# Optimization experiments

Measured on AMD Instinct MI355X. Metric: run time of the kernel, lower is better.

Reference implementation:

```python
import jax, jax.numpy as jnp
import numpy as np

EMBED = 8      # == n_qubits, forced by x[:, i, :].view(batch, n_qubits)
FFN = 4096
B, S = 32, 2048


def setup_inputs() -> dict:
    key = jax.random.key(0)
    k_x, k_t, k_w1, k_b1, k_w2, k_b2 = jax.random.split(key, 6)
    x = jax.random.normal(k_x, (B, S, EMBED), dtype=jnp.float32)
    theta = jax.random.normal(k_t, (), dtype=jnp.float32)  # shared trainable RY angle
    # torch.nn.Linear-style init bounds
    lim1 = 1.0 / np.sqrt(EMBED)
    lim2 = 1.0 / np.sqrt(FFN)
    W1 = jax.random.uniform(k_w1, (FFN, EMBED), jnp.float32, -lim1, lim1)
    b1 = jax.random.uniform(k_b1, (FFN,), jnp.float32, -lim1, lim1)
    W2 = jax.random.uniform(k_w2, (EMBED, FFN), jnp.float32, -lim2, lim2)
    b2 = jax.random.uniform(k_b2, (EMBED,), jnp.float32, -lim2, lim2)
    return {"x": x, "theta": theta, "W1": W1, "b1": b1, "W2": W2, "b2": b2}


def reference(x, theta, W1, b1, W2, b2):
    # Quantum circuit, solved analytically (product state, single-qubit gates):
    # |0> --RX(x_i)--RY(theta)--> <Z_i> = cos(theta) * cos(x_i)
    # This fuses the original per-token Python loop into one elementwise op.
    q = jnp.cos(theta) * jnp.cos(x)                 # [B, S, 8]
    # dropout is identity in eval mode
    h = jax.nn.relu(jnp.einsum('bsk,fk->bsf', q, W1) + b1)   # [B, S, FFN]
    out = jnp.einsum('bsf,ef->bse', h, W2) + b2              # [B, S, 8]
    return out
```

## Files before the change

kernel.cpp:

```cpp
#include <hip/hip_runtime.h>
#include <math.h>

#define FFN_DIM 4096
#define NCHUNK  128

typedef _Float16 f16x8 __attribute__((ext_vector_type(8)));
typedef __fp16   h16x2 __attribute__((ext_vector_type(2)));
typedef float    f32x16 __attribute__((ext_vector_type(16)));
typedef float    f32x4  __attribute__((ext_vector_type(4)));

__global__ void build_frags_kernel(const float* __restrict__ w1,
                                   const float* __restrict__ b1,
                                   const float* __restrict__ w2,
                                   _Float16* __restrict__ w1f,
                                   _Float16* __restrict__ w2f) {
    int i = blockIdx.x * 256 + threadIdx.x;
    if (i < NCHUNK * 64 * 8) {
        int j    = i & 7;
        int lane = (i >> 3) & 63;
        int cc   = i >> 9;
        _Float16 v;
        if (lane < 32) v = (_Float16)w1[(cc * 32 + lane) * 8 + j];
        else           v = (j == 0) ? (_Float16)b1[cc * 32 + (lane & 31)]
                                    : (_Float16)0.0f;
        w1f[i] = v;
    }
    if (i < NCHUNK * 2 * 16 * 8) {
        int j  = i & 7;
        int ci = (i >> 3) & 15;
        int c  = (i >> 7) & 1;
        int cc = i >> 8;
        int g = ci >> 3, e = ci & 7;
        int k = 8 * g + j;
        int fl = (k & 3) + 8 * ((k >> 2) & 1) + 4 * (k >> 3);
        int f = 32 * cc + 16 * c + fl;
        w2f[i] = (_Float16)w2[e * FFN_DIM + f];
    }
}

__global__ __launch_bounds__(256, 6) void ffq_mfma_kernel(
    const float* __restrict__ x,
    const float* __restrict__ theta,
    const _Float16* __restrict__ w1f,
    const _Float16* __restrict__ w2f,
    const float* __restrict__ b2,
    float* __restrict__ out,
    int n_tok)
{
    __shared__ float part[4][64][4];

    const int tid  = threadIdx.x;
    const int lane = tid & 63;
    const int wave = tid >> 6;
    const int l31  = lane & 31;
    const int g    = lane >> 5;

    const int tb = blockIdx.x * 32;
    const float cth = cosf(theta[0]);

    f16x8 bq = {};
    if (g == 0) {
        int tok = tb + l31;
        int rt = tok < n_tok ? tok : (n_tok - 1);
        const f32x4* xp = (const f32x4*)(x + (size_t)rt * 8);
        f32x4 x0 = xp[0], x1 = xp[1];
        bq[0] = (_Float16)(cth * cosf(x0.x));
        bq[1] = (_Float16)(cth * cosf(x0.y));
        bq[2] = (_Float16)(cth * cosf(x0.z));
        bq[3] = (_Float16)(cth * cosf(x0.w));
        bq[4] = (_Float16)(cth * cosf(x1.x));
        bq[5] = (_Float16)(cth * cosf(x1.y));
        bq[6] = (_Float16)(cth * cosf(x1.z));
        bq[7] = (_Float16)(cth * cosf(x1.w));
    } else {
        bq[0] = (_Float16)1.0f;
    }

    f32x16 acc = {};
    const f32x16 zero16 = {};

    const int  ci   = g * 8 + (l31 & 7);
    const _Float16* a1p = w1f + (size_t)lane * 8;
    const _Float16* a2p = w2f + (size_t)ci * 8;

    union U8 { f16x8 v; h16x2 p[4]; };
    const h16x2 hz = {(__fp16)0.0f, (__fp16)0.0f};

    const int c0 = wave * (NCHUNK / 4);
    const int c1 = c0 + (NCHUNK / 4);

    #pragma unroll 2
    for (int cc = c0; cc < c1; ++cc) {
        f16x8 A1  = *(const f16x8*)(a1p + (size_t)cc * 512);
        f16x8 A2a = *(const f16x8*)(a2p + (size_t)cc * 256);
        f16x8 A2b = *(const f16x8*)(a2p + (size_t)cc * 256 + 128);

        f32x16 d1 = __builtin_amdgcn_mfma_f32_32x32x16_f16(A1, bq, zero16, 0, 0, 0);

        U8 ua, ub;
        #pragma unroll
        for (int v = 0; v < 4; ++v) {
            ua.p[v] = __builtin_amdgcn_cvt_pkrtz(d1[2 * v],     d1[2 * v + 1]);
            ub.p[v] = __builtin_amdgcn_cvt_pkrtz(d1[8 + 2 * v], d1[8 + 2 * v + 1]);
        }
        #pragma unroll
        for (int v = 0; v < 4; ++v) {
            ua.p[v] = __builtin_elementwise_max(ua.p[v], hz);
            ub.p[v] = __builtin_elementwise_max(ub.p[v], hz);
        }

        acc = __builtin_amdgcn_mfma_f32_32x32x16_f16(A2a, ua.v, acc, 0, 0, 0);
        acc = __builtin_amdgcn_mfma_f32_32x32x16_f16(A2b, ub.v, acc, 0, 0, 0);
    }

    #pragma unroll
    for (int r = 0; r < 4; ++r) part[wave][lane][r] = acc[r];
    __syncthreads();

    int t = tid >> 3, e = tid & 7;
    int gt = tb + t;
    if (gt < n_tok) {
        int sl = (e >> 2) * 32 + t;
        int r  = e & 3;
        float s = part[0][sl][r] + part[1][sl][r]
                + part[2][sl][r] + part[3][sl][r] + b2[e];
        out[(size_t)gt * 8 + e] = s;
    }
}

__global__ __launch_bounds__(256, 4) void ffq_valu_kernel(
    const float* __restrict__ x, const float* __restrict__ theta,
    const float* __restrict__ w1, const float* __restrict__ b1,
    const float* __restrict__ w2, const float* __restrict__ b2,
    float* __restrict__ out, int n_tok)
{
    __shared__ float part[4][64][9];
    const int tid = threadIdx.x;
    const int lane = tid & 63;
    const int wave = __builtin_amdgcn_readfirstlane(tid >> 6);
    const int tok = blockIdx.x * 64 + lane;
    const int rtok = tok < n_tok ? tok : n_tok - 1;
    const float cth = cosf(theta[0]);
    const f32x4* xv = (const f32x4*)(x + (size_t)rtok * 8);
    f32x4 x0 = xv[0], x1 = xv[1];
    float q[8];
    q[0]=cth*cosf(x0.x); q[1]=cth*cosf(x0.y); q[2]=cth*cosf(x0.z); q[3]=cth*cosf(x0.w);
    q[4]=cth*cosf(x1.x); q[5]=cth*cosf(x1.y); q[6]=cth*cosf(x1.z); q[7]=cth*cosf(x1.w);
    float acc[8];
    #pragma unroll
    for (int e = 0; e < 8; ++e) acc[e] = 0.0f;
    const int f0 = wave * (FFN_DIM / 4), f1 = f0 + (FFN_DIM / 4);
    #pragma unroll 2
    for (int f = f0; f < f1; ++f) {
        const f32x4* w1r = (const f32x4*)(w1 + (size_t)f * 8);
        f32x4 u0 = w1r[0], u1 = w1r[1];
        float h = b1[f];
        h = fmaf(u0.x,q[0],h); h = fmaf(u0.y,q[1],h); h = fmaf(u0.z,q[2],h); h = fmaf(u0.w,q[3],h);
        h = fmaf(u1.x,q[4],h); h = fmaf(u1.y,q[5],h); h = fmaf(u1.z,q[6],h); h = fmaf(u1.w,q[7],h);
        h = fmaxf(h, 0.0f);
        #pragma unroll
        for (int e = 0; e < 8; ++e) acc[e] = fmaf(h, w2[e * FFN_DIM + f], acc[e]);
    }
    #pragma unroll
    for (int e = 0; e < 8; ++e) part[wave][lane][e] = acc[e];
    __syncthreads();
    for (int i = tid; i < 64 * 8; i += 256) {
        int t = i >> 3, e = i & 7;
        int gt = blockIdx.x * 64 + t;
        if (gt < n_tok)
            out[(size_t)gt * 8 + e] = part[0][t][e] + part[1][t][e]
                                    + part[2][t][e] + part[3][t][e] + b2[e];
    }
}

extern "C" void kernel_launch(void* const* d_in, const int* in_sizes, int n_in,
                              void* d_out, int out_size, void* d_ws, size_t ws_size,
                              hipStream_t stream) {
    const float* x     = (const float*)d_in[0];
    const float* theta = (const float*)d_in[1];
    const float* w1    = (const float*)d_in[2];
    const float* b1    = (const float*)d_in[3];
    const float* w2    = (const float*)d_in[4];
    const float* b2    = (const float*)d_in[5];
    float* out = (float*)d_out;
    const int n_tok = out_size / 8;

    const size_t W1F_BYTES = (size_t)NCHUNK * 64 * 8 * sizeof(_Float16);
    const size_t W2F_BYTES = (size_t)NCHUNK * 2 * 16 * 8 * sizeof(_Float16);

    if (ws_size >= W1F_BYTES + W2F_BYTES) {
        _Float16* w1f = (_Float16*)d_ws;
        _Float16* w2f = (_Float16*)((char*)d_ws + W1F_BYTES);
        build_frags_kernel<<<(NCHUNK * 64 * 8 + 255) / 256, 256, 0, stream>>>(
            w1, b1, w2, w1f, w2f);
        int blocks = (n_tok + 31) / 32;
        ffq_mfma_kernel<<<blocks, 256, 0, stream>>>(x, theta, w1f, w2f, b2, out,
                                                    n_tok);
    } else {
        int grid = (n_tok + 63) / 64;
        ffq_valu_kernel<<<grid, 256, 0, stream>>>(x, theta, w1, b1, w2, b2, out,
                                                  n_tok);
    }
}
```

Measured before the change: 38.98 us.

## Stage weight fragments in LDS and split FFN across blocks with reduce kernel

Each block now handles 256 tokens (8 waves of 32) over one quarter of the FFN dimension. It stages that quarter's W1/W2 fragments into shared memory once and reuses them across all waves, instead of every wave streaming its own weight slice from global or L2 memory. Partial outputs for each FFN slice go to a workspace buffer, and a new reduce kernel sums the four slices and adds b2. This trades an extra kernel launch, a partial-sum round trip through global memory and a larger workspace requirement for less repeated weight traffic.

```diff
diff --git a/kernel.cpp b/kernel.cpp
--- a/kernel.cpp
+++ b/kernel.cpp
@@ -3,6 +3,10 @@
 
 #define FFN_DIM 4096
 #define NCHUNK  128
+#define CLS     4
+#define CCHUNK  (NCHUNK / CLS)
+#define TPB     512
+#define TOKB    256
 
 typedef _Float16 f16x8 __attribute__((ext_vector_type(8)));
 typedef __fp16   h16x2 __attribute__((ext_vector_type(2)));
@@ -38,16 +42,16 @@
     }
 }
 
-__global__ __launch_bounds__(256, 6) void ffq_mfma_kernel(
+__global__ __launch_bounds__(512, 4) void ffq_mfma_kernel(
     const float* __restrict__ x,
     const float* __restrict__ theta,
     const _Float16* __restrict__ w1f,
     const _Float16* __restrict__ w2f,
-    const float* __restrict__ b2,
-    float* __restrict__ out,
+    float* __restrict__ partial,
     int n_tok)
 {
-    __shared__ float part[4][64][4];
+    __shared__ _Float16 w1s[CCHUNK][64][8];
+    __shared__ _Float16 w2s[CCHUNK][2][16][8];
 
     const int tid  = threadIdx.x;
     const int lane = tid & 63;
@@ -55,12 +59,27 @@
     const int l31  = lane & 31;
     const int g    = lane >> 5;
 
-    const int tb = blockIdx.x * 32;
+    const int cls = blockIdx.x & (CLS - 1);
+    const int tg  = blockIdx.x >> 2;
+    const int c0  = cls * CCHUNK;
+
+    {
+        const uint4* s1 = (const uint4*)(w1f + (size_t)c0 * 512);
+        uint4* d1p = (uint4*)&w1s[0][0][0];
+        #pragma unroll
+        for (int i = 0; i < (CCHUNK * 512 / 8) / TPB; ++i)
+            d1p[tid + i * TPB] = s1[tid + i * TPB];
+        const uint4* s2 = (const uint4*)(w2f + (size_t)c0 * 256);
+        uint4* d2p = (uint4*)&w2s[0][0][0][0];
+        #pragma unroll
+        for (int i = 0; i < (CCHUNK * 256 / 8) / TPB; ++i)
+            d2p[tid + i * TPB] = s2[tid + i * TPB];
+    }
+
     const float cth = cosf(theta[0]);
-
+    const int tok = tg * TOKB + wave * 32 + l31;
     f16x8 bq = {};
     if (g == 0) {
-        int tok = tb + l31;
         int rt = tok < n_tok ? tok : (n_tok - 1);
         const f32x4* xp = (const f32x4*)(x + (size_t)rt * 8);
         f32x4 x0 = xp[0], x1 = xp[1];
@@ -76,24 +95,22 @@
         bq[0] = (_Float16)1.0f;
     }
 
+    __syncthreads();
+
     f32x16 acc = {};
     const f32x16 zero16 = {};
-
-    const int  ci   = g * 8 + (l31 & 7);
-    const _Float16* a1p = w1f + (size_t)lane * 8;
-    const _Float16* a2p = w2f + (size_t)ci * 8;
+    const int ci = g * 8 + (l31 & 7);
+    const _Float16* a1p = &w1s[0][lane][0];
+    const _Float16* a2p = &w2s[0][0][ci][0];
 
     union U8 { f16x8 v; h16x2 p[4]; };
     const h16x2 hz = {(__fp16)0.0f, (__fp16)0.0f};
 
-    const int c0 = wave * (NCHUNK / 4);
-    const int c1 = c0 + (NCHUNK / 4);
-
     #pragma unroll 2
-    for (int cc = c0; cc < c1; ++cc) {
-        f16x8 A1  = *(const f16x8*)(a1p + (size_t)cc * 512);
-        f16x8 A2a = *(const f16x8*)(a2p + (size_t)cc * 256);
-        f16x8 A2b = *(const f16x8*)(a2p + (size_t)cc * 256 + 128);
+    for (int lc = 0; lc < CCHUNK; ++lc) {
+        f16x8 A1  = *(const f16x8*)(a1p + lc * 512);
+        f16x8 A2a = *(const f16x8*)(a2p + lc * 256);
+        f16x8 A2b = *(const f16x8*)(a2p + lc * 256 + 128);
 
         f32x16 d1 = __builtin_amdgcn_mfma_f32_32x32x16_f16(A1, bq, zero16, 0, 0, 0);
 
@@ -113,18 +130,27 @@
         acc = __builtin_amdgcn_mfma_f32_32x32x16_f16(A2b, ub.v, acc, 0, 0, 0);
     }
 
-    #pragma unroll
-    for (int r = 0; r < 4; ++r) part[wave][lane][r] = acc[r];
-    __syncthreads();
-
-    int t = tid >> 3, e = tid & 7;
-    int gt = tb + t;
-    if (gt < n_tok) {
-        int sl = (e >> 2) * 32 + t;
-        int r  = e & 3;
-        float s = part[0][sl][r] + part[1][sl][r]
-                + part[2][sl][r] + part[3][sl][r] + b2[e];
-        out[(size_t)gt * 8 + e] = s;
+    if (tok < n_tok) {
+        f32x4 o = {acc[0], acc[1], acc[2], acc[3]};
+        *(f32x4*)(partial + ((size_t)cls * n_tok + tok) * 8 + 4 * g) = o;
+    }
+}
+
+__global__ __launch_bounds__(256) void ffq_reduce_kernel(
+    const float* __restrict__ partial, const float* __restrict__ b2,
+    float* __restrict__ out, int n_tok)
+{
+    int j = blockIdx.x * 256 + threadIdx.x;
+    int nq = n_tok * 2;
+    if (j < nq) {
+        const f32x4* p = (const f32x4*)partial;
+        size_t stride = (size_t)n_tok * 2;
+        f32x4 s = p[j];
+        s = s + p[j + stride];
+        s = s + p[j + 2 * stride];
+        s = s + p[j + 3 * stride];
+        f32x4 bb = ((const f32x4*)b2)[j & 1];
+        ((f32x4*)out)[j] = s + bb;
     }
 }
 
@@ -187,15 +213,20 @@
 
     const size_t W1F_BYTES = (size_t)NCHUNK * 64 * 8 * sizeof(_Float16);
     const size_t W2F_BYTES = (size_t)NCHUNK * 2 * 16 * 8 * sizeof(_Float16);
-
-    if (ws_size >= W1F_BYTES + W2F_BYTES) {
+    const size_t PART_BYTES = (size_t)CLS * n_tok * 8 * sizeof(float);
+
+    if (ws_size >= W1F_BYTES + W2F_BYTES + PART_BYTES) {
         _Float16* w1f = (_Float16*)d_ws;
         _Float16* w2f = (_Float16*)((char*)d_ws + W1F_BYTES);
+        float* partial = (float*)((char*)d_ws + W1F_BYTES + W2F_BYTES);
         build_frags_kernel<<<(NCHUNK * 64 * 8 + 255) / 256, 256, 0, stream>>>(
             w1, b1, w2, w1f, w2f);
-        int blocks = (n_tok + 31) / 32;
-        ffq_mfma_kernel<<<blocks, 256, 0, stream>>>(x, theta, w1f, w2f, b2, out,
-                                                    n_tok);
+        int n_tg = (n_tok + TOKB - 1) / TOKB;
+        ffq_mfma_kernel<<<CLS * n_tg, TPB, 0, stream>>>(x, theta, w1f, w2f,
+                                                        partial, n_tok);
+        int nq = n_tok * 2;
+        ffq_reduce_kernel<<<(nq + 255) / 256, 256, 0, stream>>>(partial, b2,
+                                                                out, n_tok);
     } else {
         int grid = (n_tok + 63) / 64;
         ffq_valu_kernel<<<grid, 256, 0, stream>>>(x, theta, w1, b1, w2, b2, out,
```

After: 37.43 us. 1.04x faster.
